# Kernel tuning notes

Measured on AMD Instinct MI355X. Metric: run time of the kernel, lower is better.

## Reference

```python
import jax, jax.numpy as jnp
import numpy as np


def setup_inputs() -> dict:
    key = jax.random.key(0)
    ks = jax.random.split(key, 9)
    B, S, D = 8, 2048, 1024
    scale = 1.0 / np.sqrt(D)
    return {
        "q": jax.random.normal(ks[0], (B, S, D), jnp.float32),
        "k": jax.random.normal(ks[1], (B, S, D), jnp.float32),
        "v": jax.random.normal(ks[2], (B, S, D), jnp.float32),
        "Wq": jax.random.normal(ks[3], (D, D), jnp.float32) * scale,
        "bq": jax.random.normal(ks[4], (D,), jnp.float32) * scale,
        "Wk": jax.random.normal(ks[5], (D, D), jnp.float32) * scale,
        "bk": jax.random.normal(ks[6], (D,), jnp.float32) * scale,
        "Wv": jax.random.normal(ks[7], (D, D), jnp.float32) * scale,
        "bv": jax.random.normal(ks[8], (D,), jnp.float32) * scale,
    }


def reference(q, k, v, Wq, bq, Wk, bk, Wv, bv):
    residual = q
    # torch nn.Linear: y = x @ W^T + b
    qp = jnp.einsum('bsd,ed->bse', q, Wq) + bq
    kp = jnp.einsum('bsd,ed->bse', k, Wk) + bk
    vp = jnp.einsum('bsd,ed->bse', v, Wv) + bv
    d_k = kp.shape[-1]
    scores = jnp.einsum('bqd,bkd->bqk', qp, kp) / d_k  # non-standard: divide by d, not sqrt(d)
    # non-standard softmax over dim=1 (the QUERY axis)
    attn_probs = jax.nn.softmax(scores, axis=1)
    attn = jnp.einsum('bqk,bkd->bqd', attn_probs, vp)
    # second softmax over dim=1 (sequence axis) to produce weights
    attn_w = jax.nn.softmax(attn, axis=1)
    attn = attn + residual
    return (attn, attn_w)
```

## Files before the change

kernel.cpp:

```cpp
#include <hip/hip_runtime.h>

typedef __attribute__((ext_vector_type(2))) long lx2;
typedef __attribute__((ext_vector_type(4))) float f32x4;

__device__ __forceinline__ ushort f2bf(float f) {
  union { float f; unsigned u; } x; x.f = f;
  unsigned r = x.u + 0x7FFFu + ((x.u >> 16) & 1u);
  return (ushort)(r >> 16);
}
__device__ __forceinline__ float bf2f(ushort u) {
  union { unsigned u; float f; } x; x.u = ((unsigned)u) << 16;
  return x.f;
}

#if defined(__has_builtin)
#if __has_builtin(__builtin_amdgcn_cvt_pk_fp8_f32) && __has_builtin(__builtin_amdgcn_cvt_f32_fp8)
#define HAVE_HW_FP8 1
#endif
#endif

#ifdef HAVE_HW_FP8
__device__ __forceinline__ uint pk4_fp8(float f0, float f1, float f2, float f3) {
  int r = __builtin_amdgcn_cvt_pk_fp8_f32(f0, f1, 0, false);
  r = __builtin_amdgcn_cvt_pk_fp8_f32(f2, f3, r, true);
  return (uint)r;
}
#define FP8DEC(dw, sel) __builtin_amdgcn_cvt_f32_fp8((int)(dw), (sel))
#else
__device__ __forceinline__ unsigned char f2e4m3(float f) {
  unsigned u = __float_as_uint(f);
  unsigned s = (u >> 24) & 0x80;
  float a = fabsf(f);
  if (a != a) return (unsigned char)(s | 0x7f);
  if (a >= 448.f) return (unsigned char)(s | 0x7e);
  int ei;
  (void)frexpf(a, &ei);
  int E = ei + 6;
  if (E < 1) {
    int ki = (int)rintf(a * 512.f);
    if (ki >= 8) return (unsigned char)(s | 0x08);
    return (unsigned char)(s | ki);
  }
  float q = a * exp2f((float)(10 - E));
  int ki = (int)rintf(q);
  if (ki >= 16) { E++; ki = 8; }
  if (E > 15 || (E == 15 && ki > 14)) return (unsigned char)(s | 0x7e);
  return (unsigned char)(s | (E << 3) | (ki - 8));
}
__device__ __forceinline__ uint pk4_fp8(float f0, float f1, float f2, float f3) {
  return (uint)f2e4m3(f0) | ((uint)f2e4m3(f1) << 8) |
         ((uint)f2e4m3(f2) << 16) | ((uint)f2e4m3(f3) << 24);
}
__device__ __forceinline__ float e4m3dec(unsigned char b) {
  int E = (b >> 3) & 15, M = b & 7;
  float v = E ? ldexpf((float)(8 + M), E - 10) : ldexpf((float)M, -9);
  return (b & 0x80) ? -v : v;
}
#define FP8DEC(dw, sel) e4m3dec((unsigned char)(((dw) >> (8 * (sel))) & 0xff))
#endif

__device__ __forceinline__ void gload_lds16(const void* g, void* l) {
  __builtin_amdgcn_global_load_lds(
      (const __attribute__((address_space(1))) void*)g,
      (__attribute__((address_space(3))) void*)l, 16, 0, 0);
}

__global__ __launch_bounds__(256) void cvt3_fp8(
    const float* __restrict__ s0, const float* __restrict__ s1,
    const float* __restrict__ s2, uint* __restrict__ d0,
    uint* __restrict__ d1, uint* __restrict__ d2, long n) {
  const float* s = blockIdx.y == 0 ? s0 : (blockIdx.y == 1 ? s1 : s2);
  uint* d = blockIdx.y == 0 ? d0 : (blockIdx.y == 1 ? d1 : d2);
  const int lane = threadIdx.x & 63;
  const int w = threadIdx.x >> 6;
  const long wave_base = ((long)blockIdx.x * 4 + w) * 1024;
  if (wave_base >= n) return;
  float4 f[4];
#pragma unroll
  for (int j = 0; j < 4; ++j)
    f[j] = *(const float4*)(s + wave_base + j * 256 + lane * 4);
#pragma unroll
  for (int j = 0; j < 4; ++j)
    d[(wave_base >> 2) + j * 64 + lane] = pk4_fp8(f[j].x, f[j].y, f[j].z, f[j].w);
}

template<int BIAS_MODE, int SCALED, int REDUCE, int EXPOUT, int OUT_FP8>
__global__ __launch_bounds__(1024, 4) void gemmF(
    const unsigned char* __restrict__ A, const unsigned char* __restrict__ B,
    void* __restrict__ Cv, const float* __restrict__ bias,
    float* __restrict__ red_max, float* __restrict__ red_sum,
    int N, int K, long sA, long sB, long sC, float scale, int gm, int gn)
{
  extern __shared__ unsigned char lds[];

  const int nwg = gridDim.x;
  const int wg = blockIdx.x;
  const int cpx = nwg >> 3;
  const int wid_ = (wg & 7) * cpx + (wg >> 3);
  const int tiles = gm * gn;
  const int bz = wid_ / tiles;
  const int t2 = wid_ - bz * tiles;
  const int band = t2 / (gm << 2);
  const int r2 = t2 - band * (gm << 2);
  const int tile_m = (r2 >> 2) * 256;
  const int tile_n = ((band << 2) + (r2 & 3)) * 256;

  const unsigned char* Ab = A + (size_t)bz * sA;
  const unsigned char* Bb = B + (size_t)bz * sB;
  const int t = threadIdx.x;
  const int lane = t & 63;
  const int w = t >> 6;
  const int wr = w >> 2;
  const int wc = w & 3;

  f32x4 acc[4][4] = {};

#define STAGE(c, k0)                                                                   \
  do {                                                                                 \
    gload_lds16(Ab + (size_t)(tile_m + w * 16 + (lane & 15)) * K + (k0) +              \
                    (lane >> 4) * 16,                                                  \
                lds + (c) * 32768 + w * 1024);                                         \
    gload_lds16(Bb + (size_t)(tile_n + w * 16 + (lane & 15)) * K + (k0) +              \
                    (lane >> 4) * 16,                                                  \
                lds + (c) * 32768 + 16384 + w * 1024);                                 \
  } while (0)

  STAGE(0, 0);

  const int KT = K >> 6;
  for (int tt = 0; tt < KT; ++tt) {
    const int c = tt & 1;
    asm volatile("s_waitcnt vmcnt(0)" ::: "memory");
    __builtin_amdgcn_s_barrier();
    if (tt + 1 < KT) STAGE(c ^ 1, (tt + 1) << 6);
    lx2 aA[4], bB[4];
#pragma unroll
    for (int mi = 0; mi < 4; ++mi)
      aA[mi] = *(const lx2*)(lds + c * 32768 + (wr * 4 + mi) * 1024 + lane * 16);
#pragma unroll
    for (int nf = 0; nf < 4; ++nf)
      bB[nf] = *(const lx2*)(lds + c * 32768 + 16384 + (wc * 4 + nf) * 1024 + lane * 16);
    asm volatile("s_waitcnt lgkmcnt(0)" ::: "memory");
    __builtin_amdgcn_sched_barrier(0);
    __builtin_amdgcn_s_setprio(1);
#pragma unroll
    for (int kk = 0; kk < 2; ++kk)
#pragma unroll
      for (int mi = 0; mi < 4; ++mi)
#pragma unroll
        for (int nf = 0; nf < 4; ++nf)
          acc[mi][nf] = __builtin_amdgcn_mfma_f32_16x16x32_fp8_fp8(
              aA[mi][kk], bB[nf][kk], acc[mi][nf], 0, 0, 0);
    __builtin_amdgcn_s_setprio(0);
  }
#undef STAGE

  float sm2[4] = {0.f, 0.f, 0.f, 0.f};
  const int g5 = ((lane >> 4) & 3) << 5;
  int ccl[4]; float bcn[4];
#pragma unroll
  for (int nf = 0; nf < 4; ++nf) {
    ccl[nf] = wc * 64 + nf * 16 + (lane & 15);
    bcn[nf] = (BIAS_MODE == 1) ? bias[tile_n + ccl[nf]] : 0.f;
  }
#pragma unroll
  for (int h = 0; h < 2; ++h) {
    __syncthreads();
    if ((wr >> 1) == h) {
#pragma unroll
      for (int mi = 0; mi < 4; ++mi) {
#pragma unroll
        for (int j = 0; j < 4; ++j) {
          const int row = (wr & 1) * 64 + mi * 16 + ((lane >> 4) << 2) + j;
          float bcr = (BIAS_MODE == 2) ? bias[tile_m + h * 128 + row] : 0.f;
#pragma unroll
          for (int nf = 0; nf < 4; ++nf) {
            float val = acc[mi][nf][j];
            if (SCALED) val *= scale;
            if (BIAS_MODE == 1) val += bcn[nf];
            else if (BIAS_MODE == 2) val += bcr;
            if (EXPOUT) val = __expf(val);
            if (REDUCE == 2) sm2[nf] += val;
            *(ushort*)(lds + row * 512 + ((ccl[nf] * 2) ^ g5)) = f2bf(val);
          }
        }
      }
    }
    __syncthreads();
#pragma unroll
    for (int p = 0; p < 4; ++p) {
      int off = p * 16384 + t * 16;
      int row = off >> 9;
      int b = off & 511;
      int bs = b ^ (((row >> 2) & 3) << 5);
      f32x4 d = *(const f32x4*)(lds + row * 512 + bs);
      const int gr = tile_m + h * 128 + row;
      if (OUT_FP8) {
        const uint* dw = (const uint*)&d;
        float f0 = bf2f((ushort)(dw[0] & 0xffff)), f1 = bf2f((ushort)(dw[0] >> 16));
        float f2 = bf2f((ushort)(dw[1] & 0xffff)), f3 = bf2f((ushort)(dw[1] >> 16));
        float f4 = bf2f((ushort)(dw[2] & 0xffff)), f5 = bf2f((ushort)(dw[2] >> 16));
        float f6 = bf2f((ushort)(dw[3] & 0xffff)), f7 = bf2f((ushort)(dw[3] >> 16));
        uint2 o;
        o.x = pk4_fp8(f0, f1, f2, f3);
        o.y = pk4_fp8(f4, f5, f6, f7);
        *(uint2*)((unsigned char*)Cv + (size_t)bz * sC + (size_t)gr * N + tile_n + (b >> 1)) = o;
      } else {
        *(f32x4*)((ushort*)Cv + (size_t)bz * sC + (size_t)gr * N + tile_n + (b >> 1)) = d;
      }
    }
  }

  if constexpr (REDUCE == 2) {
    __syncthreads();
    float* sb = (float*)lds;
#pragma unroll
    for (int nf = 0; nf < 4; ++nf) {
      float s1 = sm2[nf] + __shfl_xor(sm2[nf], 16);
      float Ss = s1 + __shfl_xor(s1, 32);
      if ((lane >> 4) == nf) sb[wr * 256 + ccl[nf]] = Ss;
    }
    __syncthreads();
    if (t < 256) {
      size_t rb = ((size_t)bz * gm + (tile_m >> 8)) * N + tile_n + t;
      red_sum[rb] = sb[t] + sb[256 + t] + sb[512 + t] + sb[768 + t];
    }
  }
  if constexpr (REDUCE == 1) {
    __syncthreads();
    float* mb = (float*)lds;
    float* sb = (float*)lds + 1024;
#pragma unroll
    for (int nf = 0; nf < 4; ++nf) {
      float mx = -1e30f;
#pragma unroll
      for (int mi = 0; mi < 4; ++mi)
#pragma unroll
        for (int j = 0; j < 4; ++j) {
          float val = acc[mi][nf][j];
          if (SCALED) val *= scale;
          mx = fmaxf(mx, val);
        }
      float m1 = fmaxf(mx, __shfl_xor(mx, 16));
      float M = fmaxf(m1, __shfl_xor(m1, 32));
      float sm = 0.f;
#pragma unroll
      for (int mi = 0; mi < 4; ++mi)
#pragma unroll
        for (int j = 0; j < 4; ++j) {
          float val = acc[mi][nf][j];
          if (SCALED) val *= scale;
          sm += __expf(val - M);
        }
      float s1 = sm + __shfl_xor(sm, 16);
      float Ss = s1 + __shfl_xor(s1, 32);
      if ((lane >> 4) == nf) {
        mb[wr * 256 + ccl[nf]] = M;
        sb[wr * 256 + ccl[nf]] = Ss;
      }
    }
    __syncthreads();
    if (t < 256) {
      float M = fmaxf(fmaxf(mb[t], mb[256 + t]), fmaxf(mb[512 + t], mb[768 + t]));
      float Ss = sb[t] * __expf(mb[t] - M) + sb[256 + t] * __expf(mb[256 + t] - M) +
                 sb[512 + t] * __expf(mb[512 + t] - M) + sb[768 + t] * __expf(mb[768 + t] - M);
      size_t rb = ((size_t)bz * gm + (tile_m >> 8)) * N + tile_n + t;
      red_max[rb] = M;
      red_sum[rb] = Ss;
    }
  }
}

__global__ __launch_bounds__(256) void combine_c(
    const float* __restrict__ red_sum, float* __restrict__ cvec, int cols, int nch)
{
  const int b = blockIdx.y;
  const int c = blockIdx.x * 256 + threadIdx.x;
  float Z = 0.f;
  for (int ch = 0; ch < nch; ++ch)
    Z += red_sum[((size_t)b * nch + ch) * cols + c];
  cvec[(size_t)b * cols + c] = 1024.f / Z;
}

__global__ __launch_bounds__(256) void scale_v(
    const uint2* __restrict__ vpT, const float* __restrict__ cvec,
    uint2* __restrict__ vs, int S, long DS)
{
  const size_t i8 = (size_t)blockIdx.x * 256 + threadIdx.x;
  const size_t k8 = i8 * 8;
  const int b = (int)(k8 / DS);
  const int kcol = (int)(k8 % S);
  uint2 u = vpT[i8];
  const float* cb = cvec + (size_t)b * S + kcol;
  float f0 = FP8DEC(u.x, 0) * cb[0], f1 = FP8DEC(u.x, 1) * cb[1];
  float f2 = FP8DEC(u.x, 2) * cb[2], f3 = FP8DEC(u.x, 3) * cb[3];
  float f4 = FP8DEC(u.y, 0) * cb[4], f5 = FP8DEC(u.y, 1) * cb[5];
  float f6 = FP8DEC(u.y, 2) * cb[6], f7 = FP8DEC(u.y, 3) * cb[7];
  uint2 o;
  o.x = pk4_fp8(f0, f1, f2, f3);
  o.y = pk4_fp8(f4, f5, f6, f7);
  vs[i8] = o;
}

__global__ __launch_bounds__(256) void colsm_combine(
    const float* __restrict__ red_max, const float* __restrict__ red_sum,
    float* __restrict__ Mv, float* __restrict__ Zinv, int cols, int nch)
{
  const int b = blockIdx.y;
  const int c = blockIdx.x * 256 + threadIdx.x;
  float M = -1e30f, Z = 0.f;
  for (int ch = 0; ch < nch; ++ch) {
    size_t o = ((size_t)b * nch + ch) * cols + c;
    float m = red_max[o], s = red_sum[o];
    float nm = fmaxf(M, m);
    Z = Z * __expf(M - nm) + s * __expf(m - nm);
    M = nm;
  }
  Mv[(size_t)b * cols + c] = M;
  Zinv[(size_t)b * cols + c] = 1.f / Z;
}

__global__ __launch_bounds__(256) void final_emit(
    const ushort* __restrict__ attnB, const float* __restrict__ q,
    float* __restrict__ out0, float* __restrict__ out1,
    const float* __restrict__ Mv, const float* __restrict__ Zinv,
    int rows, int cols, int rpc)
{
  const int b = blockIdx.y;
  const int ch = blockIdx.z;
  const size_t base = (size_t)b * rows * cols;
  const int c4 = (blockIdx.x * 256 + threadIdx.x) * 4;
  const int r0 = ch * rpc;
  float M[4], Zi[4];
#pragma unroll
  for (int i = 0; i < 4; ++i) {
    M[i] = Mv[(size_t)b * cols + c4 + i];
    Zi[i] = Zinv[(size_t)b * cols + c4 + i];
  }
  for (int r = r0; r < r0 + rpc; ++r) {
    size_t o = base + (size_t)r * cols + c4;
    ushort4 u = *(const ushort4*)(attnB + o);
    float4 qv = *(const float4*)(q + o);
    float a0 = bf2f(u.x), a1 = bf2f(u.y), a2 = bf2f(u.z), a3 = bf2f(u.w);
    float4 wv, s;
    wv.x = __expf(a0 - M[0]) * Zi[0];
    wv.y = __expf(a1 - M[1]) * Zi[1];
    wv.z = __expf(a2 - M[2]) * Zi[2];
    wv.w = __expf(a3 - M[3]) * Zi[3];
    s.x = a0 + qv.x; s.y = a1 + qv.y; s.z = a2 + qv.z; s.w = a3 + qv.w;
    *(float4*)(out1 + o) = wv;
    *(float4*)(out0 + o) = s;
  }
}

extern "C" void kernel_launch(void* const* d_in, const int* in_sizes, int n_in,
                              void* d_out, int out_size, void* d_ws, size_t ws_size,
                              hipStream_t stream) {
  const float* q  = (const float*)d_in[0];
  const float* k  = (const float*)d_in[1];
  const float* v  = (const float*)d_in[2];
  const float* Wq = (const float*)d_in[3];
  const float* bq = (const float*)d_in[4];
  const float* Wk = (const float*)d_in[5];
  const float* bk = (const float*)d_in[6];
  const float* Wv = (const float*)d_in[7];
  const float* bv = (const float*)d_in[8];
  float* out = (float*)d_out;

  const int B = 8, S = 2048, D = 1024;
  const long BS = (long)B * S;
  const long nQKV = BS * D;
  const long nW = (long)D * D;

  unsigned char* qb8 = (unsigned char*)d_out;
  unsigned char* kb8 = qb8 + nQKV;
  unsigned char* vb8 = kb8 + nQKV;
  unsigned char* Wq8 = (unsigned char*)d_out + (48ull << 20);
  unsigned char* Wk8 = (unsigned char*)d_out + (49ull << 20);
  unsigned char* Wv8 = (unsigned char*)d_out + (50ull << 20);
  float* red_s_sum = (float*)((char*)d_out + (64ull << 20));
  float* c_s       = (float*)((char*)d_out + (66ull << 20));

  char* ws = (char*)d_ws;
  unsigned char* qp8   = (unsigned char*)ws;
  unsigned char* kp8   = (unsigned char*)(ws + (16ull << 20));
  unsigned char* vpT8  = (unsigned char*)(ws + (32ull << 20));
  unsigned char* vs8   = (unsigned char*)(ws + (48ull << 20));
  unsigned char* expS8 = (unsigned char*)(ws + (64ull << 20));
  ushort* attnB        = (ushort*)(ws + (96ull << 20));
  float* red_f_max = (float*)(ws + (128ull << 20));
  float* red_f_sum = (float*)(ws + (129ull << 20));
  float* Mf        = (float*)(ws + (130ull << 20));
  float* Zf        = (float*)(ws + (131ull << 20));

  const int SH = 65536;
  (void)hipFuncSetAttribute(reinterpret_cast<const void*>(&gemmF<1,0,0,0,1>),
                            hipFuncAttributeMaxDynamicSharedMemorySize, SH);
  (void)hipFuncSetAttribute(reinterpret_cast<const void*>(&gemmF<2,0,0,0,1>),
                            hipFuncAttributeMaxDynamicSharedMemorySize, SH);
  (void)hipFuncSetAttribute(reinterpret_cast<const void*>(&gemmF<0,1,2,1,1>),
                            hipFuncAttributeMaxDynamicSharedMemorySize, SH);
  (void)hipFuncSetAttribute(reinterpret_cast<const void*>(&gemmF<0,1,1,0,0>),
                            hipFuncAttributeMaxDynamicSharedMemorySize, SH);

  cvt3_fp8<<<dim3((unsigned)(nW / 4096), 3), 256, 0, stream>>>(
      Wq, Wk, Wv, (uint*)Wq8, (uint*)Wk8, (uint*)Wv8, nW);
  cvt3_fp8<<<dim3((unsigned)(nQKV / 4096), 3), 256, 0, stream>>>(
      q, k, v, (uint*)qb8, (uint*)kb8, (uint*)vb8, nQKV);

  gemmF<1,0,0,0,1><<<dim3(64 * 4), 1024, SH, stream>>>(
      qb8, Wq8, qp8, bq, nullptr, nullptr, D, D, 0, 0, 0, 1.f, 64, 4);
  gemmF<1,0,0,0,1><<<dim3(64 * 4), 1024, SH, stream>>>(
      kb8, Wk8, kp8, bk, nullptr, nullptr, D, D, 0, 0, 0, 1.f, 64, 4);
  gemmF<2,0,0,0,1><<<dim3(4 * 8 * B), 1024, SH, stream>>>(
      Wv8, vb8, vpT8, bv, nullptr, nullptr, S, D, 0, (long)S * D, (long)D * S, 1.f, 4, 8);
  gemmF<0,1,2,1,1><<<dim3(8 * 8 * B), 1024, SH, stream>>>(
      qp8, kp8, expS8, nullptr, nullptr, red_s_sum,
      S, D, (long)S * D, (long)S * D, (long)S * S, 1.f / 1024.f, 8, 8);

  combine_c<<<dim3(S / 256, B), 256, 0, stream>>>(red_s_sum, c_s, S, 8);
  scale_v<<<dim3((int)(nQKV / (256 * 8))), 256, 0, stream>>>(
      (const uint2*)vpT8, c_s, (uint2*)vs8, S, (long)D * S);

  gemmF<0,1,1,0,0><<<dim3(8 * 4 * B), 1024, SH, stream>>>(
      expS8, vs8, attnB, nullptr, red_f_max, red_f_sum,
      D, S, (long)S * S, (long)D * S, (long)S * D, 1.f / 1024.f, 8, 4);

  colsm_combine<<<dim3(D / 256, B), 256, 0, stream>>>(red_f_max, red_f_sum, Mf, Zf, D, 8);
  final_emit<<<dim3(1, B, 128), 256, 0, stream>>>(attnB, q, out, out + nQKV, Mf, Zf, S, D, 16);

  (void)in_sizes; (void)n_in; (void)out_size; (void)ws_size;
}
```

Baseline: 312.1 us.

## Fuse fp32-to-fp8 input conversion into projection GEMM operand loading

Removes the standalone conversion kernel for q, k and v and instead loads fp32 operands directly inside the projection GEMMs, converting to fp8 in registers before writing to LDS. This removes a full read/write pass over the large activation tensors and the intermediate fp8 buffers. In exchange, the GEMM main loop does synchronous register-staged loads plus conversion each K step, and reads fp32 data (4x bytes) possibly multiple times across N tiles.

```diff
diff --git a/kernel.cpp b/kernel.cpp
--- a/kernel.cpp
+++ b/kernel.cpp
@@ -84,9 +84,9 @@
     d[(wave_base >> 2) + j * 64 + lane] = pk4_fp8(f[j].x, f[j].y, f[j].z, f[j].w);
 }
 
-template<int BIAS_MODE, int SCALED, int REDUCE, int EXPOUT, int OUT_FP8>
+template<int BIAS_MODE, int SCALED, int REDUCE, int EXPOUT, int OUT_FP8, int PF32>
 __global__ __launch_bounds__(1024, 4) void gemmF(
-    const unsigned char* __restrict__ A, const unsigned char* __restrict__ B,
+    const void* __restrict__ Av, const void* __restrict__ Bv,
     void* __restrict__ Cv, const float* __restrict__ bias,
     float* __restrict__ red_max, float* __restrict__ red_sum,
     int N, int K, long sA, long sB, long sC, float scale, int gm, int gn)
@@ -105,8 +105,11 @@
   const int tile_m = (r2 >> 2) * 256;
   const int tile_n = ((band << 2) + (r2 & 3)) * 256;
 
-  const unsigned char* Ab = A + (size_t)bz * sA;
-  const unsigned char* Bb = B + (size_t)bz * sB;
+  const unsigned char* Ab8 = (PF32 == 1) ? nullptr : (const unsigned char*)Av + (size_t)bz * sA;
+  const float*         AbF = (PF32 == 1) ? (const float*)Av + (size_t)bz * sA : nullptr;
+  const unsigned char* Bb8 = (PF32 == 2) ? nullptr : (const unsigned char*)Bv + (size_t)bz * sB;
+  const float*         BbF = (PF32 == 2) ? (const float*)Bv + (size_t)bz * sB : nullptr;
+
   const int t = threadIdx.x;
   const int lane = t & 63;
   const int w = t >> 6;
@@ -114,25 +117,55 @@
   const int wc = w & 3;
 
   f32x4 acc[4][4] = {};
-
-#define STAGE(c, k0)                                                                   \
+  float4 R[4];
+
+#define STAGE_FA(c, k0)                                                                \
+    gload_lds16(Ab8 + (size_t)(tile_m + w * 16 + (lane & 15)) * K + (k0) +             \
+                    (lane >> 4) * 16,                                                  \
+                lds + (c) * 32768 + w * 1024)
+#define STAGE_FB(c, k0)                                                                \
+    gload_lds16(Bb8 + (size_t)(tile_n + w * 16 + (lane & 15)) * K + (k0) +             \
+                    (lane >> 4) * 16,                                                  \
+                lds + (c) * 32768 + 16384 + w * 1024)
+#define PLOAD(PbF, tile_p, k0)                                                         \
   do {                                                                                 \
-    gload_lds16(Ab + (size_t)(tile_m + w * 16 + (lane & 15)) * K + (k0) +              \
-                    (lane >> 4) * 16,                                                  \
-                lds + (c) * 32768 + w * 1024);                                         \
-    gload_lds16(Bb + (size_t)(tile_n + w * 16 + (lane & 15)) * K + (k0) +              \
-                    (lane >> 4) * 16,                                                  \
-                lds + (c) * 32768 + 16384 + w * 1024);                                 \
+    const float* pp = (PbF) + (size_t)((tile_p) + w * 16 + (lane & 15)) * K +          \
+                      (k0) + (lane >> 4) * 16;                                         \
+    R[0] = *(const float4*)(pp);      R[1] = *(const float4*)(pp + 4);                 \
+    R[2] = *(const float4*)(pp + 8);  R[3] = *(const float4*)(pp + 12);                \
   } while (0)
-
-  STAGE(0, 0);
+#define PWRITE(c, roff)                                                                \
+  do {                                                                                 \
+    uint4 o;                                                                           \
+    o.x = pk4_fp8(R[0].x, R[0].y, R[0].z, R[0].w);                                     \
+    o.y = pk4_fp8(R[1].x, R[1].y, R[1].z, R[1].w);                                     \
+    o.z = pk4_fp8(R[2].x, R[2].y, R[2].z, R[2].w);                                     \
+    o.w = pk4_fp8(R[3].x, R[3].y, R[3].z, R[3].w);                                     \
+    *(uint4*)(lds + (c) * 32768 + (roff) + w * 1024 + lane * 16) = o;                  \
+  } while (0)
+
+  if constexpr (PF32 == 1) { STAGE_FB(0, 0); PLOAD(AbF, tile_m, 0); }
+  else if constexpr (PF32 == 2) { STAGE_FA(0, 0); PLOAD(BbF, tile_n, 0); }
+  else { STAGE_FA(0, 0); STAGE_FB(0, 0); }
 
   const int KT = K >> 6;
   for (int tt = 0; tt < KT; ++tt) {
     const int c = tt & 1;
     asm volatile("s_waitcnt vmcnt(0)" ::: "memory");
+    if constexpr (PF32 == 1) {
+      PWRITE(c, 0);
+      asm volatile("s_waitcnt lgkmcnt(0)" ::: "memory");
+    } else if constexpr (PF32 == 2) {
+      PWRITE(c, 16384);
+      asm volatile("s_waitcnt lgkmcnt(0)" ::: "memory");
+    }
     __builtin_amdgcn_s_barrier();
-    if (tt + 1 < KT) STAGE(c ^ 1, (tt + 1) << 6);
+    if (tt + 1 < KT) {
+      const int k0n = (tt + 1) << 6;
+      if constexpr (PF32 == 1) { STAGE_FB(c ^ 1, k0n); PLOAD(AbF, tile_m, k0n); }
+      else if constexpr (PF32 == 2) { STAGE_FA(c ^ 1, k0n); PLOAD(BbF, tile_n, k0n); }
+      else { STAGE_FA(c ^ 1, k0n); STAGE_FB(c ^ 1, k0n); }
+    }
     lx2 aA[4], bB[4];
 #pragma unroll
     for (int mi = 0; mi < 4; ++mi)
@@ -153,7 +186,10 @@
               aA[mi][kk], bB[nf][kk], acc[mi][nf], 0, 0, 0);
     __builtin_amdgcn_s_setprio(0);
   }
-#undef STAGE
+#undef STAGE_FA
+#undef STAGE_FB
+#undef PLOAD
+#undef PWRITE
 
   float sm2[4] = {0.f, 0.f, 0.f, 0.f};
   const int g5 = ((lane >> 4) & 3) << 5;
@@ -372,12 +408,9 @@
   const long nQKV = BS * D;
   const long nW = (long)D * D;
 
-  unsigned char* qb8 = (unsigned char*)d_out;
-  unsigned char* kb8 = qb8 + nQKV;
-  unsigned char* vb8 = kb8 + nQKV;
-  unsigned char* Wq8 = (unsigned char*)d_out + (48ull << 20);
-  unsigned char* Wk8 = (unsigned char*)d_out + (49ull << 20);
-  unsigned char* Wv8 = (unsigned char*)d_out + (50ull << 20);
+  unsigned char* Wq8 = (unsigned char*)d_out;
+  unsigned char* Wk8 = Wq8 + nW;
+  unsigned char* Wv8 = Wk8 + nW;
   float* red_s_sum = (float*)((char*)d_out + (64ull << 20));
   float* c_s       = (float*)((char*)d_out + (66ull << 20));
 
@@ -394,27 +427,25 @@
   float* Zf        = (float*)(ws + (131ull << 20));
 
   const int SH = 65536;
-  (void)hipFuncSetAttribute(reinterpret_cast<const void*>(&gemmF<1,0,0,0,1>),
+  (void)hipFuncSetAttribute(reinterpret_cast<const void*>(&gemmF<1,0,0,0,1,1>),
                             hipFuncAttributeMaxDynamicSharedMemorySize, SH);
-  (void)hipFuncSetAttribute(reinterpret_cast<const void*>(&gemmF<2,0,0,0,1>),
+  (void)hipFuncSetAttribute(reinterpret_cast<const void*>(&gemmF<2,0,0,0,1,2>),
                             hipFuncAttributeMaxDynamicSharedMemorySize, SH);
-  (void)hipFuncSetAttribute(reinterpret_cast<const void*>(&gemmF<0,1,2,1,1>),
+  (void)hipFuncSetAttribute(reinterpret_cast<const void*>(&gemmF<0,1,2,1,1,0>),
                             hipFuncAttributeMaxDynamicSharedMemorySize, SH);
-  (void)hipFuncSetAttribute(reinterpret_cast<const void*>(&gemmF<0,1,1,0,0>),
+  (void)hipFuncSetAttribute(reinterpret_cast<const void*>(&gemmF<0,1,1,0,0,0>),
                             hipFuncAttributeMaxDynamicSharedMemorySize, SH);
 
   cvt3_fp8<<<dim3((unsigned)(nW / 4096), 3), 256, 0, stream>>>(
       Wq, Wk, Wv, (uint*)Wq8, (uint*)Wk8, (uint*)Wv8, nW);
-  cvt3_fp8<<<dim3((unsigned)(nQKV / 4096), 3), 256, 0, stream>>>(
-      q, k, v, (uint*)qb8, (uint*)kb8, (uint*)vb8, nQKV);
-
-  gemmF<1,0,0,0,1><<<dim3(64 * 4), 1024, SH, stream>>>(
-      qb8, Wq8, qp8, bq, nullptr, nullptr, D, D, 0, 0, 0, 1.f, 64, 4);
-  gemmF<1,0,0,0,1><<<dim3(64 * 4), 1024, SH, stream>>>(
-      kb8, Wk8, kp8, bk, nullptr, nullptr, D, D, 0, 0, 0, 1.f, 64, 4);
-  gemmF<2,0,0,0,1><<<dim3(4 * 8 * B), 1024, SH, stream>>>(
-      Wv8, vb8, vpT8, bv, nullptr, nullptr, S, D, 0, (long)S * D, (long)D * S, 1.f, 4, 8);
-  gemmF<0,1,2,1,1><<<dim3(8 * 8 * B), 1024, SH, stream>>>(
+
+  gemmF<1,0,0,0,1,1><<<dim3(64 * 4), 1024, SH, stream>>>(
+      q, Wq8, qp8, bq, nullptr, nullptr, D, D, 0, 0, 0, 1.f, 64, 4);
+  gemmF<1,0,0,0,1,1><<<dim3(64 * 4), 1024, SH, stream>>>(
+      k, Wk8, kp8, bk, nullptr, nullptr, D, D, 0, 0, 0, 1.f, 64, 4);
+  gemmF<2,0,0,0,1,2><<<dim3(4 * 8 * B), 1024, SH, stream>>>(
+      Wv8, v, vpT8, bv, nullptr, nullptr, S, D, 0, (long)S * D, (long)D * S, 1.f, 4, 8);
+  gemmF<0,1,2,1,1,0><<<dim3(8 * 8 * B), 1024, SH, stream>>>(
       qp8, kp8, expS8, nullptr, nullptr, red_s_sum,
       S, D, (long)S * D, (long)S * D, (long)S * S, 1.f / 1024.f, 8, 8);
 
@@ -422,7 +453,7 @@
   scale_v<<<dim3((int)(nQKV / (256 * 8))), 256, 0, stream>>>(
       (const uint2*)vpT8, c_s, (uint2*)vs8, S, (long)D * S);
 
-  gemmF<0,1,1,0,0><<<dim3(8 * 4 * B), 1024, SH, stream>>>(
+  gemmF<0,1,1,0,0,0><<<dim3(8 * 4 * B), 1024, SH, stream>>>(
       expS8, vs8, attnB, nullptr, red_f_max, red_f_sum,
       D, S, (long)S * S, (long)D * S, (long)S * D, 1.f / 1024.f, 8, 4);
 
```

Result: slower. 349.4 us (+11.9%).
